# Kernel optimization log

Measured on AMD Instinct MI355X. Metric: run time of the kernel, lower is better.

The kernel has to match this reference:

```python
import jax, jax.numpy as jnp
import numpy as np

NUM_USERS = 100000
NUM_ITEMS = 50000
EMB_DIM = 64
N_EDGES = 2000000
N_LAYERS = 3
N_NODES = NUM_USERS + NUM_ITEMS


def setup_inputs() -> dict:
    key = jax.random.key(0)
    k1, k2, k3, k4, k5 = jax.random.split(key, 5)
    user_emb = jax.random.normal(k1, (NUM_USERS, EMB_DIM), dtype=jnp.float32)
    item_emb = jax.random.normal(k2, (NUM_ITEMS, EMB_DIM), dtype=jnp.float32)
    edge_norm = jax.random.uniform(k3, (N_EDGES,), dtype=jnp.float32)
    edge_src = jax.random.randint(k4, (N_EDGES,), 0, N_NODES, dtype=jnp.int64) if jax.config.jax_enable_x64 else jax.random.randint(k4, (N_EDGES,), 0, N_NODES, dtype=jnp.int32)
    edge_dst = jax.random.randint(k5, (N_EDGES,), 0, N_NODES, dtype=edge_src.dtype)
    return {"user_emb": user_emb, "item_emb": item_emb, "edge_norm": edge_norm,
            "edge_src": edge_src, "edge_dst": edge_dst}


def reference(user_emb, item_emb, edge_norm, edge_src, edge_dst):
    # LightGCN propagation: ego[l+1][row] = sum_edges edge_norm * ego[l][col]
    ego = jnp.concatenate([user_emb, item_emb], axis=0)  # [N, D]
    acc = ego
    for _ in range(N_LAYERS):
        msg = ego[edge_dst] * edge_norm[:, None]          # [E, D] gather + scale
        ego = jax.ops.segment_sum(msg, edge_src, num_segments=N_NODES)  # scatter-add
        acc = acc + ego
    final = acc / (N_LAYERS + 1)
    return final[:NUM_USERS], final[NUM_USERS:]
```

## Files before the change

### kernel.cpp

```cpp
#include <hip/hip_runtime.h>
#include <hip/hip_fp16.h>


#define NUM_USERS 100000
#define NUM_ITEMS 50000
#define EMB_DIM   64
#define N_EDGES   2000000
#define N_NODES   (NUM_USERS + NUM_ITEMS)
#define NODE_FLOATS (N_NODES * EMB_DIM)
#define NODE_F4     (NODE_FLOATS / 4)

#define NBUCKET  512
#define NPB      293
#define NPART    8
#define NCNT     (NBUCKET * NPART)
#define BT       512
#define VPT      8
#define TILE     (BT * VPT)
#define NTILE    ((N_EDGES + TILE - 1) / TILE)

typedef unsigned int uint;
typedef unsigned short ushort;
typedef unsigned long long u64;

__device__ __forceinline__ float2 h2f2(uint u) {
    __half2 h = *reinterpret_cast<const __half2*>(&u);
    return __half22float2(h);
}
__device__ __forceinline__ uint f2h2(float a, float b) {
    __half2 h = __floats2half2_rn(a, b);
    return *reinterpret_cast<uint*>(&h);
}

__global__ void lgcn_init(const float4* __restrict__ user,
                          const float4* __restrict__ item,
                          uint2* __restrict__ egoA) {
    const int n_user4 = NUM_USERS * EMB_DIM / 4;
    for (int i = blockIdx.x * blockDim.x + threadIdx.x; i < NODE_F4;
         i += gridDim.x * blockDim.x) {
        float4 v = (i < n_user4) ? user[i] : item[i - n_user4];
        egoA[i] = make_uint2(f2h2(v.x, v.y), f2h2(v.z, v.w));
    }
}

__global__ void zero_ints(int* __restrict__ p, int n) {
    int i = blockIdx.x * blockDim.x + threadIdx.x;
    if (i < n) p[i] = 0;
}

__global__ __launch_bounds__(BT) void bucket_hist(const int* __restrict__ src,
                                                  int* __restrict__ bucketCount) {
    __shared__ int cnt[NBUCKET];
    int t = threadIdx.x;
    int part = blockIdx.x & (NPART - 1);
    cnt[t] = 0;
    __syncthreads();
    int base = blockIdx.x * TILE + t;
    #pragma unroll
    for (int k = 0; k < VPT; ++k) {
        int e = base + k * BT;
        if (e < N_EDGES) atomicAdd(&cnt[src[e] / NPB], 1);
    }
    __syncthreads();
    int c = cnt[t];
    if (c) atomicAdd(&bucketCount[t * NPART + part], c);
}

__global__ __launch_bounds__(1024) void bucket_scan(const int* __restrict__ bucketCount,
                                                    int* __restrict__ bucketOffset,
                                                    int* __restrict__ gCur,
                                                    int* __restrict__ rowPtr) {
    __shared__ int s[1024];
    int t = threadIdx.x;
    int4 c = *(const int4*)(bucketCount + t * 4);
    int sum = c.x + c.y + c.z + c.w;
    s[t] = sum;
    __syncthreads();
    for (int off = 1; off < 1024; off <<= 1) {
        int x = (t >= off) ? s[t - off] : 0;
        __syncthreads();
        s[t] += x;
        __syncthreads();
    }
    int base = s[t] - sum;
    int i0 = t * 4;
    bucketOffset[i0]     = base;
    bucketOffset[i0 + 1] = base + c.x;
    bucketOffset[i0 + 2] = base + c.x + c.y;
    bucketOffset[i0 + 3] = base + c.x + c.y + c.z;
    gCur[i0]     = base;
    gCur[i0 + 1] = base + c.x;
    gCur[i0 + 2] = base + c.x + c.y;
    gCur[i0 + 3] = base + c.x + c.y + c.z;
    if (t == 0) {
        bucketOffset[NCNT] = N_EDGES;
        rowPtr[N_NODES] = N_EDGES;
    }
}

__global__ __launch_bounds__(BT) void bucket_scatter(const int* __restrict__ src,
                                                     const int* __restrict__ dst,
                                                     const float* __restrict__ norm,
                                                     int* __restrict__ gCur,
                                                     u64* __restrict__ bpair) {
    __shared__ int cnt[NBUCKET];
    __shared__ int bbase[NBUCKET];
    int t = threadIdx.x;
    int part = blockIdx.x & (NPART - 1);
    cnt[t] = 0;
    __syncthreads();
    int base = blockIdx.x * TILE + t;
    #pragma unroll
    for (int k = 0; k < VPT; ++k) {
        int e = base + k * BT;
        if (e < N_EDGES) atomicAdd(&cnt[src[e] / NPB], 1);
    }
    __syncthreads();
    int c = cnt[t];
    bbase[t] = c ? atomicAdd(&gCur[t * NPART + part], c) : 0;
    __syncthreads();
    cnt[t] = 0;
    __syncthreads();
    #pragma unroll
    for (int k = 0; k < VPT; ++k) {
        int e = base + k * BT;
        if (e < N_EDGES) {
            int s = src[e];
            int b = s / NPB;
            int sl = s - b * NPB;
            int r = atomicAdd(&cnt[b], 1);
            uint lo = (uint)dst[e] | ((uint)sl << 18);
            u64 packed = (u64)lo | ((u64)(uint)__float_as_uint(norm[e]) << 32);
            bpair[bbase[b] + r] = packed;
        }
    }
}

__global__ __launch_bounds__(1024) void csr_finalize(const int* __restrict__ bucketOffset,
                                                     const u64* __restrict__ bpair,
                                                     int* __restrict__ rowPtr,
                                                     u64* __restrict__ pairs) {
    __shared__ int cnt[NBUCKET];
    __shared__ int cur[NBUCKET];
    int b = blockIdx.x;
    int t = threadIdx.x;
    int beg = bucketOffset[b * NPART];
    int end = bucketOffset[b * NPART + NPART];
    int nodeBase = b * NPB;

    if (t < NBUCKET) cnt[t] = 0;
    __syncthreads();
    for (int i = beg + t; i < end; i += 1024) {
        uint lo = (uint)bpair[i];
        atomicAdd(&cnt[(lo >> 18) & 0x1FF], 1);
    }
    __syncthreads();
    int v = (t < NBUCKET) ? cnt[t] : 0;
    for (int off = 1; off < NBUCKET; off <<= 1) {
        int x = (t >= off && t < NBUCKET) ? cnt[t - off] : 0;
        __syncthreads();
        if (t < NBUCKET) cnt[t] += x;
        __syncthreads();
    }
    if (t < NBUCKET) {
        int excl = cnt[t] - v;
        cur[t] = excl;
        int node = nodeBase + t;
        if (t < NPB && node < N_NODES) rowPtr[node] = beg + excl;
    }
    __syncthreads();
    for (int i = beg + t; i < end; i += 1024) {
        u64 p = bpair[i];
        int s = ((uint)p >> 18) & 0x1FF;
        int r = atomicAdd(&cur[s], 1);
        pairs[beg + r] = p;
    }
}

__global__ void lgcn_gather(const ushort* __restrict__ ego,
                            ushort* __restrict__ nego,
                            float* __restrict__ acc,
                            const ushort* __restrict__ e0,
                            const ushort* __restrict__ e1,
                            const int* __restrict__ rowPtr,
                            const u64* __restrict__ pairs,
                            int finalMode) {
    int node   = blockIdx.x * 8 + (threadIdx.x >> 5);
    int lane32 = threadIdx.x & 31;
    int g      = lane32 >> 3;
    int sub    = lane32 & 7;
    if (node >= N_NODES) return;
    int beg = rowPtr[node];
    int end = rowPtr[node + 1];

    float s0 = 0.f, s1 = 0.f, s2 = 0.f, s3 = 0.f;
    float s4 = 0.f, s5 = 0.f, s6 = 0.f, s7 = 0.f;
    for (int i = beg + g; i < end; i += 4) {
        u64 p = pairs[i];
        uint lo = (uint)p;
        float w = __uint_as_float((uint)(p >> 32));
        int d = lo & 0x3FFFF;
        uint4 r = *(const uint4*)(ego + ((size_t)d << 6) + (sub << 3));
        float2 q;
        q = h2f2(r.x); s0 += w * q.x; s1 += w * q.y;
        q = h2f2(r.y); s2 += w * q.x; s3 += w * q.y;
        q = h2f2(r.z); s4 += w * q.x; s5 += w * q.y;
        q = h2f2(r.w); s6 += w * q.x; s7 += w * q.y;
    }

    s0 += __shfl_down(s0, 16); s1 += __shfl_down(s1, 16);
    s2 += __shfl_down(s2, 16); s3 += __shfl_down(s3, 16);
    s4 += __shfl_down(s4, 16); s5 += __shfl_down(s5, 16);
    s6 += __shfl_down(s6, 16); s7 += __shfl_down(s7, 16);
    s0 += __shfl_down(s0, 8);  s1 += __shfl_down(s1, 8);
    s2 += __shfl_down(s2, 8);  s3 += __shfl_down(s3, 8);
    s4 += __shfl_down(s4, 8);  s5 += __shfl_down(s5, 8);
    s6 += __shfl_down(s6, 8);  s7 += __shfl_down(s7, 8);

    if (lane32 < 8) {
        size_t ro = ((size_t)node << 6) + (lane32 << 3);
        if (!finalMode) {
            uint4* np = (uint4*)(nego + ro);
            *np = make_uint4(f2h2(s0, s1), f2h2(s2, s3),
                             f2h2(s4, s5), f2h2(s6, s7));
        } else {
            uint4 z0 = *(const uint4*)(e0  + ro);
            uint4 z1 = *(const uint4*)(e1  + ro);
            uint4 z2 = *(const uint4*)(ego + ro);
            float2 a, b, c;
            float4 o0, o1;
            a = h2f2(z0.x); b = h2f2(z1.x); c = h2f2(z2.x);
            o0.x = (a.x + b.x + c.x + s0) * 0.25f;
            o0.y = (a.y + b.y + c.y + s1) * 0.25f;
            a = h2f2(z0.y); b = h2f2(z1.y); c = h2f2(z2.y);
            o0.z = (a.x + b.x + c.x + s2) * 0.25f;
            o0.w = (a.y + b.y + c.y + s3) * 0.25f;
            a = h2f2(z0.z); b = h2f2(z1.z); c = h2f2(z2.z);
            o1.x = (a.x + b.x + c.x + s4) * 0.25f;
            o1.y = (a.y + b.y + c.y + s5) * 0.25f;
            a = h2f2(z0.w); b = h2f2(z1.w); c = h2f2(z2.w);
            o1.z = (a.x + b.x + c.x + s6) * 0.25f;
            o1.w = (a.y + b.y + c.y + s7) * 0.25f;
            float4* ap = (float4*)(acc + ro);
            ap[0] = o0;
            ap[1] = o1;
        }
    }
}

extern "C" void kernel_launch(void* const* d_in, const int* in_sizes, int n_in,
                              void* d_out, int out_size, void* d_ws, size_t ws_size,
                              hipStream_t stream) {
    const float* user_emb  = (const float*)d_in[0];
    const float* item_emb  = (const float*)d_in[1];
    const float* edge_norm = (const float*)d_in[2];
    const int*   edge_src  = (const int*)d_in[3];
    const int*   edge_dst  = (const int*)d_in[4];
    float* acc = (float*)d_out;

    char* w = (char*)d_ws;
    ushort* egoA  = (ushort*)w;                      w += (size_t)NODE_FLOATS * 2;
    ushort* egoB  = (ushort*)w;                      w += (size_t)NODE_FLOATS * 2;
    u64*   pairs  = (u64*)w;                         w += (size_t)N_EDGES * 8;
    int*   rowPtr = (int*)w;                         w += (size_t)(N_NODES + 4) * 4;
    int*   bucketCount  = (int*)w;                   w += (size_t)NCNT * 4;
    int*   bucketOffset = (int*)w;                   w += (size_t)(NCNT + 4) * 4;
    int*   gCur   = (int*)w;                         w += (size_t)NCNT * 4;
    u64*   bpair  = (u64*)w;
    ushort* egoC  = (ushort*)w;

    const int T = 256;
    const int EW_BLOCKS = 2048;
    const int GATHER_BLOCKS = (N_NODES + 7) / 8;

    lgcn_init<<<EW_BLOCKS, T, 0, stream>>>(
        (const float4*)user_emb, (const float4*)item_emb, (uint2*)egoA);

    zero_ints<<<NCNT / T, T, 0, stream>>>(bucketCount, NCNT);
    bucket_hist<<<NTILE, BT, 0, stream>>>(edge_src, bucketCount);
    bucket_scan<<<1, 1024, 0, stream>>>(bucketCount, bucketOffset, gCur, rowPtr);
    bucket_scatter<<<NTILE, BT, 0, stream>>>(edge_src, edge_dst, edge_norm,
                                             gCur, bpair);
    csr_finalize<<<NBUCKET, 1024, 0, stream>>>(bucketOffset, bpair,
                                               rowPtr, pairs);

    lgcn_gather<<<GATHER_BLOCKS, T, 0, stream>>>(egoA, egoB, acc,
                                                 (const ushort*)0, (const ushort*)0,
                                                 rowPtr, pairs, 0);
    lgcn_gather<<<GATHER_BLOCKS, T, 0, stream>>>(egoB, egoC, acc,
                                                 (const ushort*)0, (const ushort*)0,
                                                 rowPtr, pairs, 0);
    lgcn_gather<<<GATHER_BLOCKS, T, 0, stream>>>(egoC, (ushort*)0, acc,
                                                 egoA, egoB,
                                                 rowPtr, pairs, 1);
}
```

Baseline: 345.5 us.

## Vectorize edge loads, fuse zeroing into init, stage CSR buckets in shared memory

The bucket histogram and scatter kernels now read src/dst/norm as int4/float4 with 256-thread blocks, each thread handling 8 edges. Edges are kept in registers between the counting pass and the emit pass instead of being reloaded. Zeroing of bucket counts moves into the init kernel, which removes one launch. csr_finalize stages each bucket's pairs into a 40KB shared buffer so the second pass reads LDS rather than global memory, with a fallback for buckets that overflow; the large shared allocation may lower occupancy.

```diff
diff --git a/kernel.cpp b/kernel.cpp
--- a/kernel.cpp
+++ b/kernel.cpp
@@ -14,10 +14,12 @@
 #define NPB      293
 #define NPART    8
 #define NCNT     (NBUCKET * NPART)
-#define BT       512
-#define VPT      8
-#define TILE     (BT * VPT)
-#define NTILE    ((N_EDGES + TILE - 1) / TILE)
+
+#define BT2      256
+#define NE4      (N_EDGES / 4)
+#define NT2      ((NE4 + 2 * BT2 - 1) / (2 * BT2))
+
+#define RUNCAP   5120
 
 typedef unsigned int uint;
 typedef unsigned short ushort;
@@ -34,36 +36,46 @@
 
 __global__ void lgcn_init(const float4* __restrict__ user,
                           const float4* __restrict__ item,
-                          uint2* __restrict__ egoA) {
+                          uint2* __restrict__ egoA,
+                          int* __restrict__ bucketCount) {
     const int n_user4 = NUM_USERS * EMB_DIM / 4;
-    for (int i = blockIdx.x * blockDim.x + threadIdx.x; i < NODE_F4;
-         i += gridDim.x * blockDim.x) {
+    int gid = blockIdx.x * blockDim.x + threadIdx.x;
+    if (gid < NCNT) bucketCount[gid] = 0;
+    for (int i = gid; i < NODE_F4; i += gridDim.x * blockDim.x) {
         float4 v = (i < n_user4) ? user[i] : item[i - n_user4];
         egoA[i] = make_uint2(f2h2(v.x, v.y), f2h2(v.z, v.w));
     }
 }
 
-__global__ void zero_ints(int* __restrict__ p, int n) {
-    int i = blockIdx.x * blockDim.x + threadIdx.x;
-    if (i < n) p[i] = 0;
-}
-
-__global__ __launch_bounds__(BT) void bucket_hist(const int* __restrict__ src,
-                                                  int* __restrict__ bucketCount) {
+__global__ __launch_bounds__(BT2) void bucket_hist(const int4* __restrict__ src4,
+                                                   int* __restrict__ bucketCount) {
     __shared__ int cnt[NBUCKET];
     int t = threadIdx.x;
     int part = blockIdx.x & (NPART - 1);
     cnt[t] = 0;
-    __syncthreads();
-    int base = blockIdx.x * TILE + t;
-    #pragma unroll
-    for (int k = 0; k < VPT; ++k) {
-        int e = base + k * BT;
-        if (e < N_EDGES) atomicAdd(&cnt[src[e] / NPB], 1);
-    }
-    __syncthreads();
-    int c = cnt[t];
-    if (c) atomicAdd(&bucketCount[t * NPART + part], c);
+    cnt[t + 256] = 0;
+    __syncthreads();
+    int i0 = blockIdx.x * (2 * BT2) + t;
+    int i1 = i0 + BT2;
+    if (i0 < NE4) {
+        int4 s = src4[i0];
+        atomicAdd(&cnt[s.x / NPB], 1);
+        atomicAdd(&cnt[s.y / NPB], 1);
+        atomicAdd(&cnt[s.z / NPB], 1);
+        atomicAdd(&cnt[s.w / NPB], 1);
+    }
+    if (i1 < NE4) {
+        int4 s = src4[i1];
+        atomicAdd(&cnt[s.x / NPB], 1);
+        atomicAdd(&cnt[s.y / NPB], 1);
+        atomicAdd(&cnt[s.z / NPB], 1);
+        atomicAdd(&cnt[s.w / NPB], 1);
+    }
+    __syncthreads();
+    int c0 = cnt[t];
+    int c1 = cnt[t + 256];
+    if (c0) atomicAdd(&bucketCount[t * NPART + part], c0);
+    if (c1) atomicAdd(&bucketCount[(t + 256) * NPART + part], c1);
 }
 
 __global__ __launch_bounds__(1024) void bucket_scan(const int* __restrict__ bucketCount,
@@ -98,42 +110,64 @@
     }
 }
 
-__global__ __launch_bounds__(BT) void bucket_scatter(const int* __restrict__ src,
-                                                     const int* __restrict__ dst,
-                                                     const float* __restrict__ norm,
-                                                     int* __restrict__ gCur,
-                                                     u64* __restrict__ bpair) {
+__global__ __launch_bounds__(BT2) void bucket_scatter(const int4* __restrict__ src4,
+                                                      const int4* __restrict__ dst4,
+                                                      const float4* __restrict__ norm4,
+                                                      int* __restrict__ gCur,
+                                                      u64* __restrict__ bpair) {
     __shared__ int cnt[NBUCKET];
     __shared__ int bbase[NBUCKET];
     int t = threadIdx.x;
     int part = blockIdx.x & (NPART - 1);
     cnt[t] = 0;
-    __syncthreads();
-    int base = blockIdx.x * TILE + t;
-    #pragma unroll
-    for (int k = 0; k < VPT; ++k) {
-        int e = base + k * BT;
-        if (e < N_EDGES) atomicAdd(&cnt[src[e] / NPB], 1);
-    }
-    __syncthreads();
-    int c = cnt[t];
-    bbase[t] = c ? atomicAdd(&gCur[t * NPART + part], c) : 0;
+    cnt[t + 256] = 0;
+    __syncthreads();
+    int i0 = blockIdx.x * (2 * BT2) + t;
+    int i1 = i0 + BT2;
+    bool va = i0 < NE4, vb = i1 < NE4;
+    int4 sa, sb, da, db;
+    float4 na, nb;
+    if (va) {
+        sa = src4[i0]; da = dst4[i0]; na = norm4[i0];
+        atomicAdd(&cnt[sa.x / NPB], 1);
+        atomicAdd(&cnt[sa.y / NPB], 1);
+        atomicAdd(&cnt[sa.z / NPB], 1);
+        atomicAdd(&cnt[sa.w / NPB], 1);
+    }
+    if (vb) {
+        sb = src4[i1]; db = dst4[i1]; nb = norm4[i1];
+        atomicAdd(&cnt[sb.x / NPB], 1);
+        atomicAdd(&cnt[sb.y / NPB], 1);
+        atomicAdd(&cnt[sb.z / NPB], 1);
+        atomicAdd(&cnt[sb.w / NPB], 1);
+    }
+    __syncthreads();
+    int c0 = cnt[t];
+    int c1 = cnt[t + 256];
+    bbase[t]       = c0 ? atomicAdd(&gCur[t * NPART + part], c0) : 0;
+    bbase[t + 256] = c1 ? atomicAdd(&gCur[(t + 256) * NPART + part], c1) : 0;
     __syncthreads();
     cnt[t] = 0;
-    __syncthreads();
-    #pragma unroll
-    for (int k = 0; k < VPT; ++k) {
-        int e = base + k * BT;
-        if (e < N_EDGES) {
-            int s = src[e];
-            int b = s / NPB;
-            int sl = s - b * NPB;
-            int r = atomicAdd(&cnt[b], 1);
-            uint lo = (uint)dst[e] | ((uint)sl << 18);
-            u64 packed = (u64)lo | ((u64)(uint)__float_as_uint(norm[e]) << 32);
-            bpair[bbase[b] + r] = packed;
-        }
-    }
+    cnt[t + 256] = 0;
+    __syncthreads();
+
+    #define EMIT(S, D, W) {                                             \
+        int b_ = (S) / NPB;                                             \
+        int sl_ = (S) - b_ * NPB;                                       \
+        int r_ = atomicAdd(&cnt[b_], 1);                                \
+        uint lo_ = (uint)(D) | ((uint)sl_ << 18);                       \
+        bpair[bbase[b_] + r_] =                                         \
+            (u64)lo_ | ((u64)(uint)__float_as_uint(W) << 32);           \
+    }
+    if (va) {
+        EMIT(sa.x, da.x, na.x); EMIT(sa.y, da.y, na.y);
+        EMIT(sa.z, da.z, na.z); EMIT(sa.w, da.w, na.w);
+    }
+    if (vb) {
+        EMIT(sb.x, db.x, nb.x); EMIT(sb.y, db.y, nb.y);
+        EMIT(sb.z, db.z, nb.z); EMIT(sb.w, db.w, nb.w);
+    }
+    #undef EMIT
 }
 
 __global__ __launch_bounds__(1024) void csr_finalize(const int* __restrict__ bucketOffset,
@@ -142,17 +176,28 @@
                                                      u64* __restrict__ pairs) {
     __shared__ int cnt[NBUCKET];
     __shared__ int cur[NBUCKET];
+    __shared__ u64 run[RUNCAP];
     int b = blockIdx.x;
     int t = threadIdx.x;
     int beg = bucketOffset[b * NPART];
     int end = bucketOffset[b * NPART + NPART];
+    int n = end - beg;
     int nodeBase = b * NPB;
+    bool staged = (n <= RUNCAP);
 
     if (t < NBUCKET) cnt[t] = 0;
     __syncthreads();
-    for (int i = beg + t; i < end; i += 1024) {
-        uint lo = (uint)bpair[i];
-        atomicAdd(&cnt[(lo >> 18) & 0x1FF], 1);
+    if (staged) {
+        for (int i = t; i < n; i += 1024) {
+            u64 p = bpair[beg + i];
+            run[i] = p;
+            atomicAdd(&cnt[((uint)p >> 18) & 0x1FF], 1);
+        }
+    } else {
+        for (int i = beg + t; i < end; i += 1024) {
+            uint lo = (uint)bpair[i];
+            atomicAdd(&cnt[(lo >> 18) & 0x1FF], 1);
+        }
     }
     __syncthreads();
     int v = (t < NBUCKET) ? cnt[t] : 0;
@@ -169,11 +214,20 @@
         if (t < NPB && node < N_NODES) rowPtr[node] = beg + excl;
     }
     __syncthreads();
-    for (int i = beg + t; i < end; i += 1024) {
-        u64 p = bpair[i];
-        int s = ((uint)p >> 18) & 0x1FF;
-        int r = atomicAdd(&cur[s], 1);
-        pairs[beg + r] = p;
+    if (staged) {
+        for (int i = t; i < n; i += 1024) {
+            u64 p = run[i];
+            int s = ((uint)p >> 18) & 0x1FF;
+            int r = atomicAdd(&cur[s], 1);
+            pairs[beg + r] = p;
+        }
+    } else {
+        for (int i = beg + t; i < end; i += 1024) {
+            u64 p = bpair[i];
+            int s = ((uint)p >> 18) & 0x1FF;
+            int r = atomicAdd(&cur[s], 1);
+            pairs[beg + r] = p;
+        }
     }
 }
 
@@ -274,13 +328,15 @@
     const int GATHER_BLOCKS = (N_NODES + 7) / 8;
 
     lgcn_init<<<EW_BLOCKS, T, 0, stream>>>(
-        (const float4*)user_emb, (const float4*)item_emb, (uint2*)egoA);
-
-    zero_ints<<<NCNT / T, T, 0, stream>>>(bucketCount, NCNT);
-    bucket_hist<<<NTILE, BT, 0, stream>>>(edge_src, bucketCount);
+        (const float4*)user_emb, (const float4*)item_emb, (uint2*)egoA,
+        bucketCount);
+
+    bucket_hist<<<NT2, BT2, 0, stream>>>((const int4*)edge_src, bucketCount);
     bucket_scan<<<1, 1024, 0, stream>>>(bucketCount, bucketOffset, gCur, rowPtr);
-    bucket_scatter<<<NTILE, BT, 0, stream>>>(edge_src, edge_dst, edge_norm,
-                                             gCur, bpair);
+    bucket_scatter<<<NT2, BT2, 0, stream>>>((const int4*)edge_src,
+                                            (const int4*)edge_dst,
+                                            (const float4*)edge_norm,
+                                            gCur, bpair);
     csr_finalize<<<NBUCKET, 1024, 0, stream>>>(bucketOffset, bpair,
                                                rowPtr, pairs);
 
```

Result: slower. 362.9 us (+5.0%).
